# Optimization experiments

Measured on AMD Instinct MI355X. Metric: run time of the kernel, lower is better.

Reference implementation:

```python
import jax, jax.numpy as jnp
import numpy as np

B, S, NV, D = 2, 4096, 8, 256
E = 256          # embedding dim for adaLN conditioning
H = 8            # D / n_head_channels(=32)
HID = 4 * D      # ResLayer MLP hidden
EPS = 1e-5


def setup_inputs() -> dict:
    key = jax.random.key(0)
    ks = jax.random.split(key, 16)
    M = NV * D

    def w(k, shape, scale=0.02):
        return jax.random.normal(k, shape, dtype=jnp.float32) * scale

    mask = jax.random.uniform(ks[0], (B, S, NV)) > 0.2
    mask = mask.at[..., 0].set(True)  # avoid fully-masked rows
    return {
        "x": jax.random.normal(ks[1], (B, S, NV, D), dtype=jnp.float32),
        "emb": jax.random.normal(ks[2], (B, E), dtype=jnp.float32),
        "mask": mask,
        "w_mod1": w(ks[3], (E, 2 * M)), "b_mod1": jnp.zeros((2 * M,), jnp.float32),
        "wq": w(ks[4], (D, D)), "bq": jnp.zeros((D,), jnp.float32),
        "wk": w(ks[5], (D, D)), "bk": jnp.zeros((D,), jnp.float32),
        "wv": w(ks[6], (D, D)), "bv": jnp.zeros((D,), jnp.float32),
        "wo": w(ks[7], (D, D)), "bo": jnp.zeros((D,), jnp.float32),
        "gamma": jnp.full((D,), 1e-6, jnp.float32),
        "w_mod2": w(ks[8], (E, 2 * M)), "b_mod2": jnp.zeros((2 * M,), jnp.float32),
        "w1": w(ks[9], (D, HID)), "b1": jnp.zeros((HID,), jnp.float32),
        "w2": w(ks[10], (HID, D)), "b2": jnp.zeros((D,), jnp.float32),
        "gamma_mlp": jnp.full((D,), 1e-6, jnp.float32),
    }


def _adaln(xin, emb, w, b):
    # AdaptiveLayerNorm over the flattened (NV*D) feature dims,
    # scale/shift conditioned on the embedding.
    b_, s_, nv_, d_ = xin.shape
    xf = xin.reshape(b_, s_, nv_ * d_)
    mu = xf.mean(-1, keepdims=True)
    var = ((xf - mu) ** 2).mean(-1, keepdims=True)
    normed = (xf - mu) * jax.lax.rsqrt(var + EPS)
    scale, shift = jnp.split(emb @ w + b, 2, axis=-1)  # [B, NV*D] each
    out = normed * (1.0 + scale[:, None, :]) + shift[:, None, :]
    return out.reshape(b_, s_, nv_, d_)


def reference(x, emb, mask, w_mod1, b_mod1, wq, bq, wk, bk, wv, bv, wo, bo,
              gamma, w_mod2, b_mod2, w1, b1, w2, b2, gamma_mlp):
    b_, s_, nv_, d_ = x.shape
    hd = d_ // H
    inv_sqrt = jnp.float32(1.0 / np.sqrt(hd))

    # --- attention branch: adaLN -> shape_to_att -> masked attention over variables ---
    h = _adaln(x, emb, w_mod1, b_mod1).reshape(b_ * s_, nv_, d_)
    q = (h @ wq + bq).reshape(b_ * s_, nv_, H, hd)
    k = (h @ wk + bk).reshape(b_ * s_, nv_, H, hd)
    v = (h @ wv + bv).reshape(b_ * s_, nv_, H, hd)
    scores = jnp.einsum('bnhd,bmhd->bhnm', q, k) * inv_sqrt  # [B*S, H, NV, NV]
    mk = mask.reshape(b_ * s_, nv_)
    scores = jnp.where(mk[:, None, None, :], scores, jnp.float32(-1e9))
    attn = jax.nn.softmax(scores, axis=-1)
    o = jnp.einsum('bhnm,bmhd->bnhd', attn, v).reshape(b_ * s_, nv_, d_)
    o = o @ wo + bo
    # dropout is identity at eval; gamma-scaled residual add
    x1 = x + gamma * o.reshape(b_, s_, nv_, d_)

    # --- MLP branch: shape_to_x -> adaLN -> shape_to_att -> ResLayer -> gamma residual ---
    h2 = _adaln(x1, emb, w_mod2, b_mod2)
    m = jax.nn.gelu(h2 @ w1 + b1) @ w2 + b2
    return x1 + gamma_mlp * m
```

## Files before the change

kernel.cpp:

```cpp
#include <hip/hip_runtime.h>
#include <hip/hip_bf16.h>
#include <stdint.h>

#define S_TOK   8192
#define MFEAT   2048

typedef __attribute__((ext_vector_type(4))) float f32x4;
typedef __attribute__((ext_vector_type(8))) short bf16x8;

__device__ __forceinline__ float b2f(uint32_t u) { return __uint_as_float(u << 16); }
__device__ __forceinline__ uint16_t f2b(float f) {
  uint32_t u = __float_as_uint(f);
  uint32_t r = u + 0x7fffu + ((u >> 16) & 1u);
  return (uint16_t)(r >> 16);
}
__device__ __forceinline__ uint32_t pk_bf16(float lo, float hi) {
  uint32_t r;
  asm("v_cvt_pk_bf16_f32 %0, %1, %2" : "=v"(r) : "v"(lo), "v"(hi));
  return r;
}

#define GLP(p) ((__attribute__((address_space(1))) void*)(uintptr_t)(p))
#define LDSP(p) ((__attribute__((address_space(3))) void*)(p))

__global__ __launch_bounds__(256) void k_maskprobe(const uint32_t* __restrict__ m,
                                                   int* __restrict__ flag) {
  __shared__ int s[5];
  const int tid = threadIdx.x;
  if (tid < 5) s[tid] = (tid == 4) ? 0 : 1;
  __syncthreads();
  bool i32ok = true, i8ok = true, f32ok = true, bf16ok = true, saw = false;
  for (int i = tid; i < 1024; i += 256) {
    uint32_t w = m[i];
    if (w > 1u) i32ok = false;
    if (((w | (w >> 8) | (w >> 16) | (w >> 24)) & 0xFEu) != 0) i8ok = false;
    if (w != 0u && w != 0x3F800000u) f32ok = false;
    uint32_t h0 = w & 0xffffu, h1 = w >> 16;
    if ((h0 != 0u && h0 != 0x3F80u) || (h1 != 0u && h1 != 0x3F80u)) bf16ok = false;
    if (w == 0x3F803F80u) saw = true;
  }
  if (!i32ok) s[0] = 0;
  if (!i8ok)  s[1] = 0;
  if (!f32ok) s[2] = 0;
  if (!bf16ok) s[3] = 0;
  if (saw)    s[4] = 1;
  __syncthreads();
  if (tid == 0) {
    int f;
    if (s[0]) f = 0;
    else if (s[1]) f = 1;
    else if (s[3] && s[4]) f = 3;
    else if (s[2]) f = 2;
    else if (s[3]) f = 3;
    else f = 0;
    *flag = f;
  }
}

__global__ __launch_bounds__(256) void k_prep(
    const float* __restrict__ wq, const float* __restrict__ wk,
    const float* __restrict__ wv, const float* __restrict__ wo,
    const float* __restrict__ w1, const float* __restrict__ w2,
    uint16_t* __restrict__ wqf, uint16_t* __restrict__ wof,
    uint16_t* __restrict__ w1f, uint16_t* __restrict__ w2f,
    const void* __restrict__ mask, const int* __restrict__ flag,
    int* __restrict__ mask_i32,
    const float* __restrict__ bq, const float* __restrict__ bk,
    const float* __restrict__ bv, float* __restrict__ biasqkv) {
  int idx = blockIdx.x * 256 + threadIdx.x;
  if (idx < 196608) {
    int o = idx, frag = o >> 9, lane = (o >> 3) & 63, sub = o & 7;
    int ct = frag >> 3, kt = frag & 7;
    int col = ct * 16 + (lane & 15);
    int k = kt * 32 + (lane >> 4) * 8 + sub;
    const float* src = (col < 256) ? wq : (col < 512) ? wk : wv;
    wqf[idx] = f2b(src[k * 256 + (col & 255)]);
  } else if (idx < 262144) {
    int o = idx - 196608, frag = o >> 9, lane = (o >> 3) & 63, sub = o & 7;
    int ct = frag >> 3, kt = frag & 7;
    int col = ct * 16 + (lane & 15);
    int k = kt * 32 + (lane >> 4) * 8 + sub;
    wof[o] = f2b(wo[k * 256 + col]);
  } else if (idx < 524288) {
    int o = idx - 262144, frag = o >> 9, lane = (o >> 3) & 63, sub = o & 7;
    int ct = frag >> 3, kt = frag & 7;
    int col = ct * 16 + (lane & 15);
    int k = kt * 32 + (lane >> 4) * 8 + sub;
    w1f[o] = f2b(w1[k * 1024 + col]);
  } else if (idx < 786432) {
    int o = idx - 524288, frag = o >> 9, lane = (o >> 3) & 63, sub = o & 7;
    int ct = frag >> 5, kt = frag & 31;
    int col = ct * 16 + (lane & 15);
    int k = kt * 32 + (lane >> 4) * 8 + sub;
    w2f[o] = f2b(w2[k * 256 + col]);
  } else if (idx < 851968) {
    int i = idx - 786432;
    int f = *flag;
    int v;
    if (f == 0)      v = ((const int*)mask)[i] != 0;
    else if (f == 1) v = ((const uint8_t*)mask)[i] != 0;
    else if (f == 2) v = ((const uint32_t*)mask)[i] != 0;
    else             v = ((const uint16_t*)mask)[i] != 0;
    mask_i32[i] = v;
  } else if (idx < 852736) {
    int i = idx - 851968;
    biasqkv[i] = (i < 256) ? bq[i] : (i < 512) ? bk[i - 256] : bv[i - 512];
  }
}

__global__ __launch_bounds__(256) void k_mods(
    const float* __restrict__ emb,
    const float* __restrict__ w_mod1, const float* __restrict__ b_mod1,
    const float* __restrict__ w_mod2, const float* __restrict__ b_mod2,
    float* __restrict__ mods) {
  const int j = blockIdx.x * 256 + threadIdx.x;
  const int b = blockIdx.y;
  const int which = blockIdx.z;
  const float* w  = which ? w_mod2 : w_mod1;
  const float* bb = which ? b_mod2 : b_mod1;
  __shared__ float e[256];
  e[threadIdx.x] = emb[b * 256 + threadIdx.x];
  __syncthreads();
  float acc = bb[j];
  for (int kx = 0; kx < 256; kx++) acc += e[kx] * w[(size_t)kx * 4096 + j];
  mods[((size_t)which * 2 + b) * 4096 + j] = acc;
}

__global__ __launch_bounds__(256) void k_qkv(
    const float* __restrict__ x, const float* __restrict__ mods,
    const float* __restrict__ biasqkv, const uint16_t* __restrict__ wqf,
    uint16_t* __restrict__ out, size_t slot, int t0) {
  __shared__ __align__(16) uint16_t As[128 * 256];
  __shared__ float red1[256], red2[256];
  const int tid = threadIdx.x;
  const int l = tid & 63;
  const int wva = tid >> 6;
  const int wr = wva >> 1, wc = wva & 1;
  const int brow = blockIdx.x * 128;
  char* AsB = (char*)As;

  {
    const int r = tid >> 1, ch = (tid & 1) << 7;
    const float4* xp = (const float4*)(x + (size_t)(brow + r) * 256 + ch);
    float s1 = 0.f, s2 = 0.f;
#pragma unroll
    for (int i = 0; i < 32; i++) {
      float4 u = xp[i];
      s1 += u.x + u.y + u.z + u.w;
      s2 += u.x * u.x + u.y * u.y + u.z * u.z + u.w * u.w;
    }
    red1[tid] = s1; red2[tid] = s2;
  }
  __syncthreads();
  {
    const int r = tid >> 1;
    const int base = (r >> 3) << 4;
    float s1 = 0.f, s2 = 0.f;
#pragma unroll
    for (int i = 0; i < 16; i++) { s1 += red1[base + i]; s2 += red2[base + i]; }
    float mean = s1 * (1.f / 2048.f);
    float var = s2 * (1.f / 2048.f) - mean * mean;
    float rs = rsqrtf(var + 1e-5f);
    __syncthreads();
    red1[r] = mean; red2[r] = rs;
  }
  __syncthreads();

#pragma unroll
  for (int it = 0; it < 16; it++) {
    int cidx = it * 256 + tid;
    int row = cidx >> 5, cg = cidx & 31;
    int b = (t0 + ((brow + row) >> 3)) >> 12;
    const float* mo = mods + (size_t)b * 4096 + ((row & 7) << 8) + cg * 8;
    float mean = red1[row], rs = red2[row];
    const float4* xp = (const float4*)(x + (size_t)(brow + row) * 256 + cg * 8);
    float4 u0 = xp[0], u1 = xp[1];
    float4 c0 = *(const float4*)mo,        c1 = *(const float4*)(mo + 4);
    float4 h0 = *(const float4*)(mo + 2048), h1 = *(const float4*)(mo + 2052);
    float v[8] = {u0.x,u0.y,u0.z,u0.w,u1.x,u1.y,u1.z,u1.w};
    float sc[8] = {c0.x,c0.y,c0.z,c0.w,c1.x,c1.y,c1.z,c1.w};
    float sh[8] = {h0.x,h0.y,h0.z,h0.w,h1.x,h1.y,h1.z,h1.w};
    uint32_t w[4];
#pragma unroll
    for (int i = 0; i < 4; i++) {
      float y0 = (v[i*2]   - mean) * rs * (1.f + sc[i*2])   + sh[i*2];
      float y1 = (v[i*2+1] - mean) * rs * (1.f + sc[i*2+1]) + sh[i*2+1];
      w[i] = pk_bf16(y0, y1);
    }
    *(uint4*)(AsB + row * 512 + ((cg * 16) ^ ((row & 7) << 4))) =
        make_uint4(w[0], w[1], w[2], w[3]);
  }
  __syncthreads();

#pragma unroll 1
  for (int nb = 0; nb < 6; nb++) {
    f32x4 acc[4][4];
#pragma unroll
    for (int m = 0; m < 4; m++)
#pragma unroll
      for (int n = 0; n < 4; n++) acc[m][n] = (f32x4)0.f;

#pragma unroll
    for (int kt = 0; kt < 8; kt++) {
      bf16x8 a[4], b[4];
#pragma unroll
      for (int n = 0; n < 4; n++) {
        int ct = nb * 8 + wc * 4 + n;
        b[n] = *(const bf16x8*)(wqf + (((size_t)ct * 8 + kt) * 64 + l) * 8);
      }
#pragma unroll
      for (int m = 0; m < 4; m++) {
        int row = wr * 64 + m * 16 + (l & 15);
        int cb = (kt * 64 + (l >> 4) * 16) ^ ((row & 7) << 4);
        a[m] = *(const bf16x8*)(AsB + row * 512 + cb);
      }
#pragma unroll
      for (int m = 0; m < 4; m++)
#pragma unroll
        for (int n = 0; n < 4; n++)
          acc[m][n] = __builtin_amdgcn_mfma_f32_16x16x32_bf16(a[m], b[n], acc[m][n], 0, 0, 0);
    }

#pragma unroll
    for (int m = 0; m < 4; m++) {
#pragma unroll
      for (int n = 0; n < 4; n++) {
        int col = nb * 128 + wc * 64 + n * 16 + (l & 15);
        float bc = biasqkv[col];
        int b_ = col >> 8, coll = col & 255;
#pragma unroll
        for (int r = 0; r < 4; r++) {
          int row = brow + wr * 64 + m * 16 + (l >> 4) * 4 + r;
          out[(size_t)b_ * slot + (size_t)row * 256 + coll] = f2b(acc[m][n][r] + bc);
        }
      }
    }
  }
}

__global__ __launch_bounds__(256) void k_oproj(
    const uint16_t* __restrict__ A, const uint16_t* __restrict__ wof,
    const float* __restrict__ bias, const float* __restrict__ res,
    const float* __restrict__ gam, uint16_t* __restrict__ x1b,
    float* __restrict__ sbuf) {
  __shared__ __align__(16) uint16_t As[128 * 256];
  __shared__ float sr1[16][2], sr2[16][2];
  const int tid = threadIdx.x;
  const int l = tid & 63;
  const int wva = tid >> 6;
  const int wr = wva >> 1, wc = wva & 1;
  const int brow = blockIdx.x * 128;
  char* AsB = (char*)As;

#pragma unroll
  for (int i = 0; i < 16; i++) {
    int chunk = wva * 16 + i;
    int r = chunk * 2 + (l >> 5);
    int sb = ((l & 31) * 16) ^ ((r & 7) << 4);
    __builtin_amdgcn_global_load_lds(GLP(A + (size_t)(brow + r) * 256 + (sb >> 1)),
                                     LDSP(AsB + chunk * 1024), 16, 0, 0);
  }
  asm volatile("s_waitcnt vmcnt(0)" ::: "memory");
  __syncthreads();

  float ts1[4] = {0.f, 0.f, 0.f, 0.f}, ts2[4] = {0.f, 0.f, 0.f, 0.f};

#pragma unroll 1
  for (int nb = 0; nb < 2; nb++) {
    f32x4 acc[4][4];
#pragma unroll
    for (int m = 0; m < 4; m++)
#pragma unroll
      for (int n = 0; n < 4; n++) acc[m][n] = (f32x4)0.f;

#pragma unroll
    for (int kt = 0; kt < 8; kt++) {
      bf16x8 a[4], b[4];
#pragma unroll
      for (int n = 0; n < 4; n++) {
        int ct = nb * 8 + wc * 4 + n;
        b[n] = *(const bf16x8*)(wof + (((size_t)ct * 8 + kt) * 64 + l) * 8);
      }
#pragma unroll
      for (int m = 0; m < 4; m++) {
        int row = wr * 64 + m * 16 + (l & 15);
        int cb = (kt * 64 + (l >> 4) * 16) ^ ((row & 7) << 4);
        a[m] = *(const bf16x8*)(AsB + row * 512 + cb);
      }
#pragma unroll
      for (int m = 0; m < 4; m++)
#pragma unroll
        for (int n = 0; n < 4; n++)
          acc[m][n] = __builtin_amdgcn_mfma_f32_16x16x32_bf16(a[m], b[n], acc[m][n], 0, 0, 0);
    }

#pragma unroll
    for (int m = 0; m < 4; m++) {
#pragma unroll
      for (int n = 0; n < 4; n++) {
        int col = nb * 128 + wc * 64 + n * 16 + (l & 15);
        float bc = bias[col];
        float gc = gam[col];
#pragma unroll
        for (int r = 0; r < 4; r++) {
          int row = brow + wr * 64 + m * 16 + (l >> 4) * 4 + r;
          float y = res[(size_t)row * 256 + col] + gc * (acc[m][n][r] + bc);
          x1b[(size_t)row * 256 + col] = f2b(y);
          ts1[m] += y; ts2[m] += y * y;
        }
      }
    }
  }

#pragma unroll
  for (int m = 0; m < 4; m++) {
#pragma unroll
    for (int off = 16; off; off >>= 1) {
      ts1[m] += __shfl_xor(ts1[m], off);
      ts2[m] += __shfl_xor(ts2[m], off);
    }
  }
  if ((l & 31) == 0) {
    int h = l >> 5;
#pragma unroll
    for (int m = 0; m < 4; m++) {
      int tok = wr * 8 + 2 * m + h;
      sr1[tok][wc] = ts1[m]; sr2[tok][wc] = ts2[m];
    }
  }
  __syncthreads();
  if (tid < 16) {
    float s1 = sr1[tid][0] + sr1[tid][1];
    float s2 = sr2[tid][0] + sr2[tid][1];
    float mean = s1 * (1.f / 2048.f);
    float var = s2 * (1.f / 2048.f) - mean * mean;
    sbuf[((brow >> 3) + tid) * 2]     = mean;
    sbuf[((brow >> 3) + tid) * 2 + 1] = rsqrtf(var + 1e-5f);
  }
}

__global__ __launch_bounds__(256) void k_mlp(
    const uint16_t* __restrict__ x1b, float* __restrict__ outp,
    const float* __restrict__ mods, const float* __restrict__ sbuf,
    const uint16_t* __restrict__ w1f, const float* __restrict__ b1,
    const uint16_t* __restrict__ w2f, const float* __restrict__ b2,
    const float* __restrict__ gam, int t0) {
  __shared__ __align__(16) uint16_t As[64 * 256];
  __shared__ __align__(16) uint16_t Hs[64 * 128];
  const int tid = threadIdx.x;
  const int l = tid & 63;
  const int w = tid >> 6;
  const int brow = blockIdx.x * 64;
  char* AsB = (char*)As;
  char* HsB = (char*)Hs;

#pragma unroll
  for (int it = 0; it < 8; it++) {
    int cidx = it * 256 + tid;
    int row = cidx >> 5, cg = cidx & 31;
    int gtok = (brow + row) >> 3;
    int b = (t0 + gtok) >> 12;
    const float* mo = mods + (size_t)b * 4096 + ((row & 7) << 8) + cg * 8;
    float mean = sbuf[gtok * 2], rs = sbuf[gtok * 2 + 1];
    uint4 u = *(const uint4*)(x1b + (size_t)(brow + row) * 256 + cg * 8);
    float v[8] = {b2f(u.x & 0xffff), b2f(u.x >> 16), b2f(u.y & 0xffff), b2f(u.y >> 16),
                  b2f(u.z & 0xffff), b2f(u.z >> 16), b2f(u.w & 0xffff), b2f(u.w >> 16)};
    float4 c0 = *(const float4*)mo,        c1 = *(const float4*)(mo + 4);
    float4 h0 = *(const float4*)(mo + 2048), h1 = *(const float4*)(mo + 2052);
    float sc[8] = {c0.x,c0.y,c0.z,c0.w,c1.x,c1.y,c1.z,c1.w};
    float sh[8] = {h0.x,h0.y,h0.z,h0.w,h1.x,h1.y,h1.z,h1.w};
    uint32_t wv[4];
#pragma unroll
    for (int i = 0; i < 4; i++) {
      float y0 = (v[i*2]   - mean) * rs * (1.f + sc[i*2])   + sh[i*2];
      float y1 = (v[i*2+1] - mean) * rs * (1.f + sc[i*2+1]) + sh[i*2+1];
      wv[i] = pk_bf16(y0, y1);
    }
    *(uint4*)(AsB + row * 512 + ((cg * 16) ^ ((row & 7) << 4))) =
        make_uint4(wv[0], wv[1], wv[2], wv[3]);
  }

  f32x4 acc2[4][4];
#pragma unroll
  for (int m = 0; m < 4; m++)
#pragma unroll
    for (int n = 0; n < 4; n++) acc2[m][n] = (f32x4)0.f;
  __syncthreads();

#pragma unroll 1
  for (int c = 0; c < 8; c++) {
    f32x4 acc1[2][4];
#pragma unroll
    for (int n = 0; n < 2; n++)
#pragma unroll
      for (int m = 0; m < 4; m++) acc1[n][m] = (f32x4)0.f;
#pragma unroll
    for (int kt = 0; kt < 8; kt++) {
      bf16x8 a[4], b[2];
#pragma unroll
      for (int n = 0; n < 2; n++) {
        int ct = c * 8 + w * 2 + n;
        b[n] = *(const bf16x8*)(w1f + (((size_t)ct * 8 + kt) * 64 + l) * 8);
      }
#pragma unroll
      for (int m = 0; m < 4; m++) {
        int row = m * 16 + (l & 15);
        int cb = (kt * 64 + (l >> 4) * 16) ^ ((row & 7) << 4);
        a[m] = *(const bf16x8*)(AsB + row * 512 + cb);
      }
#pragma unroll
      for (int n = 0; n < 2; n++)
#pragma unroll
        for (int m = 0; m < 4; m++)
          acc1[n][m] = __builtin_amdgcn_mfma_f32_16x16x32_bf16(b[n], a[m], acc1[n][m], 0, 0, 0);
    }
    __syncthreads();
#pragma unroll
    for (int n = 0; n < 2; n++) {
      int hb = w * 32 + n * 16 + (l >> 4) * 4;
      float4 bb = *(const float4*)(b1 + c * 128 + hb);
#pragma unroll
      for (int m = 0; m < 4; m++) {
        int token = m * 16 + (l & 15);
        float g[4];
#pragma unroll
        for (int j = 0; j < 4; j++) {
          float y = acc1[n][m][j] + ((const float*)&bb)[j];
          float t = __expf(-1.702f * y);
          g[j] = __fdividef(y, 1.f + t);
        }
        int byte = (token * 256 + hb * 2) ^ ((token & 7) << 4);
        *(uint2*)(HsB + byte) = make_uint2(pk_bf16(g[0], g[1]), pk_bf16(g[2], g[3]));
      }
    }
    __syncthreads();
#pragma unroll
    for (int kt = 0; kt < 4; kt++) {
      bf16x8 h[4], b[4];
#pragma unroll
      for (int n = 0; n < 4; n++) {
        int ct = w * 4 + n;
        int kidx = c * 4 + kt;
        b[n] = *(const bf16x8*)(w2f + (((size_t)ct * 32 + kidx) * 64 + l) * 8);
      }
#pragma unroll
      for (int m = 0; m < 4; m++) {
        int row = m * 16 + (l & 15);
        int cb = (kt * 64 + (l >> 4) * 16) ^ ((row & 7) << 4);
        h[m] = *(const bf16x8*)(HsB + row * 256 + cb);
      }
#pragma unroll
      for (int m = 0; m < 4; m++)
#pragma unroll
        for (int n = 0; n < 4; n++)
          acc2[m][n] = __builtin_amdgcn_mfma_f32_16x16x32_bf16(h[m], b[n], acc2[m][n], 0, 0, 0);
    }
  }

#pragma unroll
  for (int m = 0; m < 4; m++) {
#pragma unroll
    for (int n = 0; n < 4; n++) {
      int col = w * 64 + n * 16 + (l & 15);
      float bc = b2[col];
      float gc = gam[col];
#pragma unroll
      for (int r = 0; r < 4; r++) {
        int row = brow + m * 16 + (l >> 4) * 4 + r;
        float y = b2f(x1b[(size_t)row * 256 + col]) + gc * (acc2[m][n][r] + bc);
        outp[(size_t)row * 256 + col] = y;
      }
    }
  }
}

__global__ __launch_bounds__(256) void k_attn(
    const uint16_t* __restrict__ q, const uint16_t* __restrict__ k,
    const uint16_t* __restrict__ v, const int* __restrict__ mask,
    uint16_t* __restrict__ o) {
  __shared__ __align__(16) uint16_t kk[4][2048];
  __shared__ __align__(16) uint16_t vv[4][2048];
  const int l = threadIdx.x & 63;
  const int wva = threadIdx.x >> 6;
  const int t = blockIdx.x * 4 + wva;

#pragma unroll
  for (int c = 0; c < 4; c++) {
    __builtin_amdgcn_global_load_lds(GLP(k + (size_t)t * 2048 + c * 512 + l * 8),
                                     LDSP(&kk[wva][c * 512]), 16, 0, 0);
    __builtin_amdgcn_global_load_lds(GLP(v + (size_t)t * 2048 + c * 512 + l * 8),
                                     LDSP(&vv[wva][c * 512]), 16, 0, 0);
  }

  const int h = l >> 3, n = l & 7;
  const uint4* qp = (const uint4*)(q + (size_t)t * 2048 + n * 256 + h * 32);
  float qf[32];
#pragma unroll
  for (int c = 0; c < 4; c++) {
    uint4 u = qp[c];
    qf[c*8+0]=b2f(u.x & 0xffff); qf[c*8+1]=b2f(u.x >> 16);
    qf[c*8+2]=b2f(u.y & 0xffff); qf[c*8+3]=b2f(u.y >> 16);
    qf[c*8+4]=b2f(u.z & 0xffff); qf[c*8+5]=b2f(u.z >> 16);
    qf[c*8+6]=b2f(u.w & 0xffff); qf[c*8+7]=b2f(u.w >> 16);
  }
  asm volatile("s_waitcnt vmcnt(0)" ::: "memory");

  float s[8];
#pragma unroll
  for (int m = 0; m < 8; m++) {
    const uint4* kp = (const uint4*)&kk[wva][m * 256 + h * 32];
    float acc = 0.f;
#pragma unroll
    for (int c = 0; c < 4; c++) {
      uint4 u = kp[c];
      acc += qf[c*8+0]*b2f(u.x & 0xffff) + qf[c*8+1]*b2f(u.x >> 16)
           + qf[c*8+2]*b2f(u.y & 0xffff) + qf[c*8+3]*b2f(u.y >> 16)
           + qf[c*8+4]*b2f(u.z & 0xffff) + qf[c*8+5]*b2f(u.z >> 16)
           + qf[c*8+6]*b2f(u.w & 0xffff) + qf[c*8+7]*b2f(u.w >> 16);
    }
    s[m] = acc * 0.17677669529663687f;
  }
  const int* mk = mask + (size_t)t * 8;
  float mx = -1e30f;
#pragma unroll
  for (int m = 0; m < 8; m++) { s[m] = mk[m] ? s[m] : -1e9f; mx = fmaxf(mx, s[m]); }
  float p[8], sum = 0.f;
#pragma unroll
  for (int m = 0; m < 8; m++) { p[m] = __expf(s[m] - mx); sum += p[m]; }
  float inv = __fdividef(1.f, sum);
  float of[32];
#pragma unroll
  for (int d = 0; d < 32; d++) of[d] = 0.f;
#pragma unroll
  for (int m = 0; m < 8; m++) {
    float pm = p[m] * inv;
    const uint4* vp = (const uint4*)&vv[wva][m * 256 + h * 32];
#pragma unroll
    for (int c = 0; c < 4; c++) {
      uint4 u = vp[c];
      of[c*8+0]+=pm*b2f(u.x & 0xffff); of[c*8+1]+=pm*b2f(u.x >> 16);
      of[c*8+2]+=pm*b2f(u.y & 0xffff); of[c*8+3]+=pm*b2f(u.y >> 16);
      of[c*8+4]+=pm*b2f(u.z & 0xffff); of[c*8+5]+=pm*b2f(u.z >> 16);
      of[c*8+6]+=pm*b2f(u.w & 0xffff); of[c*8+7]+=pm*b2f(u.w >> 16);
    }
  }
  uint16_t* op = o + (size_t)t * 2048 + n * 256 + h * 32;
#pragma unroll
  for (int c = 0; c < 4; c++) {
    ((uint4*)op)[c] = make_uint4(pk_bf16(of[c*8+0], of[c*8+1]),
                                 pk_bf16(of[c*8+2], of[c*8+3]),
                                 pk_bf16(of[c*8+4], of[c*8+5]),
                                 pk_bf16(of[c*8+6], of[c*8+7]));
  }
}

extern "C" void kernel_launch(void* const* d_in, const int* in_sizes, int n_in,
                              void* d_out, int out_size, void* d_ws, size_t ws_size,
                              hipStream_t stream) {
  const float* x      = (const float*)d_in[0];
  const float* emb    = (const float*)d_in[1];
  const void*  mask   = d_in[2];
  const float* w_mod1 = (const float*)d_in[3];
  const float* b_mod1 = (const float*)d_in[4];
  const float* wq = (const float*)d_in[5];
  const float* bq = (const float*)d_in[6];
  const float* wk = (const float*)d_in[7];
  const float* bk = (const float*)d_in[8];
  const float* wv = (const float*)d_in[9];
  const float* bv = (const float*)d_in[10];
  const float* wo = (const float*)d_in[11];
  const float* bo = (const float*)d_in[12];
  const float* gamma     = (const float*)d_in[13];
  const float* w_mod2    = (const float*)d_in[14];
  const float* b_mod2    = (const float*)d_in[15];
  const float* w1 = (const float*)d_in[16];
  const float* b1 = (const float*)d_in[17];
  const float* w2 = (const float*)d_in[18];
  const float* b2 = (const float*)d_in[19];
  const float* gamma_mlp = (const float*)d_in[20];

  char* ws = (char*)d_ws;
  float*    mods = (float*)ws;
  uint16_t* wqf = (uint16_t*)(ws + 65536);
  uint16_t* wof = wqf + 196608;
  uint16_t* w1f = wof + 65536;
  uint16_t* w2f = w1f + 262144;
  int*      mask_i32 = (int*)(w2f + 262144);
  int*      flag = mask_i32 + 65536;
  float*    biasqkv = (float*)(flag + 1);
  float*    sbuf = biasqkv + 768;
  uint16_t* slots = (uint16_t*)(ws + (2u << 20));
  float*    xout = (float*)d_out;

  size_t budget = (ws_size > (3u << 20)) ? ws_size - (2u << 20) : 0;
  int maxtok = (int)(budget / 20480);
  int chunk_tokens = 16;
  for (int c = 8192; c >= 16; c >>= 1) { if (c <= maxtok) { chunk_tokens = c; break; } }
  const int nchunks = S_TOK / chunk_tokens;
  const int crows = chunk_tokens * 8;
  const size_t slot = (size_t)crows * 256;
  uint16_t* C0 = slots;
  uint16_t* C1 = C0 + slot;
  uint16_t* C4 = C0 + 4 * slot;

  k_maskprobe<<<dim3(1), 256, 0, stream>>>((const uint32_t*)mask, flag);
  k_prep<<<dim3(3331), 256, 0, stream>>>(wq, wk, wv, wo, w1, w2, wqf, wof, w1f, w2f,
                                         mask, flag, mask_i32, bq, bk, bv, biasqkv);
  k_mods<<<dim3(16, 2, 2), 256, 0, stream>>>(emb, w_mod1, b_mod1, w_mod2, b_mod2, mods);

  for (int c = 0; c < nchunks; c++) {
    const int t0 = c * chunk_tokens;
    const size_t eo = (size_t)t0 * MFEAT;
    const float* xc = x + eo;
    float* outc = xout + eo;
    k_qkv<<<dim3(crows / 128), 256, 0, stream>>>(xc, mods, biasqkv, wqf, C1, slot, t0);
    k_attn<<<dim3(chunk_tokens / 4), 256, 0, stream>>>(C1, C1 + slot, C1 + 2 * slot,
                                                       mask_i32 + (size_t)t0 * 8, C0);
    k_oproj<<<dim3(crows / 128), 256, 0, stream>>>(C0, wof, bo, xc, gamma, C4, sbuf);
    k_mlp<<<dim3(crows / 64), 256, 0, stream>>>(C4, outc, mods + 2 * 4096, sbuf,
                                                w1f, b1, w2f, b2, gamma_mlp, t0);
  }
}
```

Before: 288.9 us.

## Fuse variable attention into output projection kernel via shared LDS tile

Merges the attention kernel and the output-projection kernel into one kernel. Each 64-row block (8 tokens) loads K and V into LDS, computes masked softmax attention per wave, and writes the attention output back into the same LDS buffer in a swizzled layout. The MFMA O-projection then reads that buffer directly, which removes the global write and re-read of the attention output and one launch per chunk. In exchange the projection tile shrinks from 128 to 64 rows with 4 waves splitting columns, so wof weight reuse per block drops and the grid doubles.

Result: slower. 317.6 us (+9.9%).

```diff
diff --git a/kernel.cpp b/kernel.cpp
--- a/kernel.cpp
+++ b/kernel.cpp
@@ -238,73 +238,132 @@
   }
 }
 
-__global__ __launch_bounds__(256) void k_oproj(
-    const uint16_t* __restrict__ A, const uint16_t* __restrict__ wof,
-    const float* __restrict__ bias, const float* __restrict__ res,
-    const float* __restrict__ gam, uint16_t* __restrict__ x1b,
-    float* __restrict__ sbuf) {
-  __shared__ __align__(16) uint16_t As[128 * 256];
-  __shared__ float sr1[16][2], sr2[16][2];
+__global__ __launch_bounds__(256) void k_oav(
+    const uint16_t* __restrict__ q, const uint16_t* __restrict__ kk,
+    const uint16_t* __restrict__ vv, const int* __restrict__ mask,
+    const uint16_t* __restrict__ wof, const float* __restrict__ bias,
+    const float* __restrict__ res, const float* __restrict__ gam,
+    uint16_t* __restrict__ x1b, float* __restrict__ sbuf) {
+  __shared__ __align__(16) uint16_t As[8 * 4096];
+  __shared__ float sr1[8][4], sr2[8][4];
   const int tid = threadIdx.x;
   const int l = tid & 63;
-  const int wva = tid >> 6;
-  const int wr = wva >> 1, wc = wva & 1;
-  const int brow = blockIdx.x * 128;
+  const int w = tid >> 6;
+  const int brow = blockIdx.x * 64;
+  const int T0 = brow >> 3;
   char* AsB = (char*)As;
 
 #pragma unroll
   for (int i = 0; i < 16; i++) {
-    int chunk = wva * 16 + i;
-    int r = chunk * 2 + (l >> 5);
-    int sb = ((l & 31) * 16) ^ ((r & 7) << 4);
-    __builtin_amdgcn_global_load_lds(GLP(A + (size_t)(brow + r) * 256 + (sb >> 1)),
-                                     LDSP(AsB + chunk * 1024), 16, 0, 0);
+    int chunk = w * 16 + i;
+    int tl = chunk >> 3, sub = chunk & 7;
+    const uint16_t* src = ((sub < 4) ? kk : vv) + (size_t)(T0 + tl) * 2048 + (sub & 3) * 512;
+    __builtin_amdgcn_global_load_lds(GLP(src + l * 8), LDSP(AsB + chunk * 1024), 16, 0, 0);
   }
   asm volatile("s_waitcnt vmcnt(0)" ::: "memory");
+
+  const int h = l >> 3, n = l & 7;
+#pragma unroll 1
+  for (int tl2 = 0; tl2 < 2; tl2++) {
+    const int tl = w * 2 + tl2;
+    const uint4* qp = (const uint4*)(q + (size_t)(T0 + tl) * 2048 + n * 256 + h * 32);
+    float qf[32];
+#pragma unroll
+    for (int c = 0; c < 4; c++) {
+      uint4 u = qp[c];
+      qf[c*8+0]=b2f(u.x & 0xffff); qf[c*8+1]=b2f(u.x >> 16);
+      qf[c*8+2]=b2f(u.y & 0xffff); qf[c*8+3]=b2f(u.y >> 16);
+      qf[c*8+4]=b2f(u.z & 0xffff); qf[c*8+5]=b2f(u.z >> 16);
+      qf[c*8+6]=b2f(u.w & 0xffff); qf[c*8+7]=b2f(u.w >> 16);
+    }
+    float s[8];
+#pragma unroll
+    for (int m = 0; m < 8; m++) {
+      const uint4* kp = (const uint4*)(AsB + tl * 8192 + m * 512 + h * 64);
+      float acc = 0.f;
+#pragma unroll
+      for (int c = 0; c < 4; c++) {
+        uint4 u = kp[c];
+        acc += qf[c*8+0]*b2f(u.x & 0xffff) + qf[c*8+1]*b2f(u.x >> 16)
+             + qf[c*8+2]*b2f(u.y & 0xffff) + qf[c*8+3]*b2f(u.y >> 16)
+             + qf[c*8+4]*b2f(u.z & 0xffff) + qf[c*8+5]*b2f(u.z >> 16)
+             + qf[c*8+6]*b2f(u.w & 0xffff) + qf[c*8+7]*b2f(u.w >> 16);
+      }
+      s[m] = acc * 0.17677669529663687f;
+    }
+    const int* mk = mask + (size_t)(T0 + tl) * 8;
+    float mx = -1e30f;
+#pragma unroll
+    for (int m = 0; m < 8; m++) { s[m] = mk[m] ? s[m] : -1e9f; mx = fmaxf(mx, s[m]); }
+    float p[8], sum = 0.f;
+#pragma unroll
+    for (int m = 0; m < 8; m++) { p[m] = __expf(s[m] - mx); sum += p[m]; }
+    float inv = __fdividef(1.f, sum);
+    float of[32];
+#pragma unroll
+    for (int d = 0; d < 32; d++) of[d] = 0.f;
+#pragma unroll
+    for (int m = 0; m < 8; m++) {
+      float pm = p[m] * inv;
+      const uint4* vp = (const uint4*)(AsB + tl * 8192 + 4096 + m * 512 + h * 64);
+#pragma unroll
+      for (int c = 0; c < 4; c++) {
+        uint4 u = vp[c];
+        of[c*8+0]+=pm*b2f(u.x & 0xffff); of[c*8+1]+=pm*b2f(u.x >> 16);
+        of[c*8+2]+=pm*b2f(u.y & 0xffff); of[c*8+3]+=pm*b2f(u.y >> 16);
+        of[c*8+4]+=pm*b2f(u.z & 0xffff); of[c*8+5]+=pm*b2f(u.z >> 16);
+        of[c*8+6]+=pm*b2f(u.w & 0xffff); of[c*8+7]+=pm*b2f(u.w >> 16);
+      }
+    }
+#pragma unroll
+    for (int c = 0; c < 4; c++) {
+      int byte = tl * 8192 + n * 512 + ((h * 64 + c * 16) ^ (n << 4));
+      *(uint4*)(AsB + byte) = make_uint4(pk_bf16(of[c*8+0], of[c*8+1]),
+                                         pk_bf16(of[c*8+2], of[c*8+3]),
+                                         pk_bf16(of[c*8+4], of[c*8+5]),
+                                         pk_bf16(of[c*8+6], of[c*8+7]));
+    }
+  }
   __syncthreads();
 
   float ts1[4] = {0.f, 0.f, 0.f, 0.f}, ts2[4] = {0.f, 0.f, 0.f, 0.f};
-
 #pragma unroll 1
   for (int nb = 0; nb < 2; nb++) {
-    f32x4 acc[4][4];
-#pragma unroll
-    for (int m = 0; m < 4; m++)
-#pragma unroll
-      for (int n = 0; n < 4; n++) acc[m][n] = (f32x4)0.f;
-
+    f32x4 acc[4][2];
+#pragma unroll
+    for (int m = 0; m < 4; m++) { acc[m][0] = (f32x4)0.f; acc[m][1] = (f32x4)0.f; }
 #pragma unroll
     for (int kt = 0; kt < 8; kt++) {
-      bf16x8 a[4], b[4];
-#pragma unroll
-      for (int n = 0; n < 4; n++) {
-        int ct = nb * 8 + wc * 4 + n;
-        b[n] = *(const bf16x8*)(wof + (((size_t)ct * 8 + kt) * 64 + l) * 8);
+      bf16x8 a[4], b[2];
+#pragma unroll
+      for (int n2 = 0; n2 < 2; n2++) {
+        int ct = w * 4 + nb * 2 + n2;
+        b[n2] = *(const bf16x8*)(wof + (((size_t)ct * 8 + kt) * 64 + l) * 8);
       }
 #pragma unroll
       for (int m = 0; m < 4; m++) {
-        int row = wr * 64 + m * 16 + (l & 15);
-        int cb = (kt * 64 + (l >> 4) * 16) ^ ((row & 7) << 4);
-        a[m] = *(const bf16x8*)(AsB + row * 512 + cb);
+        int row = m * 16 + (l & 15);
+        int byte = (row >> 3) * 8192 + (row & 7) * 512 +
+                   ((kt * 64 + (l >> 4) * 16) ^ ((row & 7) << 4));
+        a[m] = *(const bf16x8*)(AsB + byte);
       }
 #pragma unroll
       for (int m = 0; m < 4; m++)
 #pragma unroll
-        for (int n = 0; n < 4; n++)
-          acc[m][n] = __builtin_amdgcn_mfma_f32_16x16x32_bf16(a[m], b[n], acc[m][n], 0, 0, 0);
-    }
-
+        for (int n2 = 0; n2 < 2; n2++)
+          acc[m][n2] = __builtin_amdgcn_mfma_f32_16x16x32_bf16(a[m], b[n2], acc[m][n2], 0, 0, 0);
+    }
 #pragma unroll
     for (int m = 0; m < 4; m++) {
 #pragma unroll
-      for (int n = 0; n < 4; n++) {
-        int col = nb * 128 + wc * 64 + n * 16 + (l & 15);
+      for (int n2 = 0; n2 < 2; n2++) {
+        int col = w * 64 + nb * 32 + n2 * 16 + (l & 15);
         float bc = bias[col];
         float gc = gam[col];
 #pragma unroll
         for (int r = 0; r < 4; r++) {
-          int row = brow + wr * 64 + m * 16 + (l >> 4) * 4 + r;
-          float y = res[(size_t)row * 256 + col] + gc * (acc[m][n][r] + bc);
+          int row = brow + m * 16 + (l >> 4) * 4 + r;
+          float y = res[(size_t)row * 256 + col] + gc * (acc[m][n2][r] + bc);
           x1b[(size_t)row * 256 + col] = f2b(y);
           ts1[m] += y; ts2[m] += y * y;
         }
@@ -321,21 +380,21 @@
     }
   }
   if ((l & 31) == 0) {
-    int h = l >> 5;
+    int hh = l >> 5;
 #pragma unroll
     for (int m = 0; m < 4; m++) {
-      int tok = wr * 8 + 2 * m + h;
-      sr1[tok][wc] = ts1[m]; sr2[tok][wc] = ts2[m];
-    }
-  }
-  __syncthreads();
-  if (tid < 16) {
-    float s1 = sr1[tid][0] + sr1[tid][1];
-    float s2 = sr2[tid][0] + sr2[tid][1];
+      int tok = 2 * m + hh;
+      sr1[tok][w] = ts1[m]; sr2[tok][w] = ts2[m];
+    }
+  }
+  __syncthreads();
+  if (tid < 8) {
+    float s1 = sr1[tid][0] + sr1[tid][1] + sr1[tid][2] + sr1[tid][3];
+    float s2 = sr2[tid][0] + sr2[tid][1] + sr2[tid][2] + sr2[tid][3];
     float mean = s1 * (1.f / 2048.f);
     float var = s2 * (1.f / 2048.f) - mean * mean;
-    sbuf[((brow >> 3) + tid) * 2]     = mean;
-    sbuf[((brow >> 3) + tid) * 2 + 1] = rsqrtf(var + 1e-5f);
+    sbuf[(T0 + tid) * 2]     = mean;
+    sbuf[(T0 + tid) * 2 + 1] = rsqrtf(var + 1e-5f);
   }
 }
 
@@ -471,86 +530,6 @@
         outp[(size_t)row * 256 + col] = y;
       }
     }
-  }
-}
-
-__global__ __launch_bounds__(256) void k_attn(
-    const uint16_t* __restrict__ q, const uint16_t* __restrict__ k,
-    const uint16_t* __restrict__ v, const int* __restrict__ mask,
-    uint16_t* __restrict__ o) {
-  __shared__ __align__(16) uint16_t kk[4][2048];
-  __shared__ __align__(16) uint16_t vv[4][2048];
-  const int l = threadIdx.x & 63;
-  const int wva = threadIdx.x >> 6;
-  const int t = blockIdx.x * 4 + wva;
-
-#pragma unroll
-  for (int c = 0; c < 4; c++) {
-    __builtin_amdgcn_global_load_lds(GLP(k + (size_t)t * 2048 + c * 512 + l * 8),
-                                     LDSP(&kk[wva][c * 512]), 16, 0, 0);
-    __builtin_amdgcn_global_load_lds(GLP(v + (size_t)t * 2048 + c * 512 + l * 8),
-                                     LDSP(&vv[wva][c * 512]), 16, 0, 0);
-  }
-
-  const int h = l >> 3, n = l & 7;
-  const uint4* qp = (const uint4*)(q + (size_t)t * 2048 + n * 256 + h * 32);
-  float qf[32];
-#pragma unroll
-  for (int c = 0; c < 4; c++) {
-    uint4 u = qp[c];
-    qf[c*8+0]=b2f(u.x & 0xffff); qf[c*8+1]=b2f(u.x >> 16);
-    qf[c*8+2]=b2f(u.y & 0xffff); qf[c*8+3]=b2f(u.y >> 16);
-    qf[c*8+4]=b2f(u.z & 0xffff); qf[c*8+5]=b2f(u.z >> 16);
-    qf[c*8+6]=b2f(u.w & 0xffff); qf[c*8+7]=b2f(u.w >> 16);
-  }
-  asm volatile("s_waitcnt vmcnt(0)" ::: "memory");
-
-  float s[8];
-#pragma unroll
-  for (int m = 0; m < 8; m++) {
-    const uint4* kp = (const uint4*)&kk[wva][m * 256 + h * 32];
-    float acc = 0.f;
-#pragma unroll
-    for (int c = 0; c < 4; c++) {
-      uint4 u = kp[c];
-      acc += qf[c*8+0]*b2f(u.x & 0xffff) + qf[c*8+1]*b2f(u.x >> 16)
-           + qf[c*8+2]*b2f(u.y & 0xffff) + qf[c*8+3]*b2f(u.y >> 16)
-           + qf[c*8+4]*b2f(u.z & 0xffff) + qf[c*8+5]*b2f(u.z >> 16)
-           + qf[c*8+6]*b2f(u.w & 0xffff) + qf[c*8+7]*b2f(u.w >> 16);
-    }
-    s[m] = acc * 0.17677669529663687f;
-  }
-  const int* mk = mask + (size_t)t * 8;
-  float mx = -1e30f;
-#pragma unroll
-  for (int m = 0; m < 8; m++) { s[m] = mk[m] ? s[m] : -1e9f; mx = fmaxf(mx, s[m]); }
-  float p[8], sum = 0.f;
-#pragma unroll
-  for (int m = 0; m < 8; m++) { p[m] = __expf(s[m] - mx); sum += p[m]; }
-  float inv = __fdividef(1.f, sum);
-  float of[32];
-#pragma unroll
-  for (int d = 0; d < 32; d++) of[d] = 0.f;
-#pragma unroll
-  for (int m = 0; m < 8; m++) {
-    float pm = p[m] * inv;
-    const uint4* vp = (const uint4*)&vv[wva][m * 256 + h * 32];
-#pragma unroll
-    for (int c = 0; c < 4; c++) {
-      uint4 u = vp[c];
-      of[c*8+0]+=pm*b2f(u.x & 0xffff); of[c*8+1]+=pm*b2f(u.x >> 16);
-      of[c*8+2]+=pm*b2f(u.y & 0xffff); of[c*8+3]+=pm*b2f(u.y >> 16);
-      of[c*8+4]+=pm*b2f(u.z & 0xffff); of[c*8+5]+=pm*b2f(u.z >> 16);
-      of[c*8+6]+=pm*b2f(u.w & 0xffff); of[c*8+7]+=pm*b2f(u.w >> 16);
-    }
-  }
-  uint16_t* op = o + (size_t)t * 2048 + n * 256 + h * 32;
-#pragma unroll
-  for (int c = 0; c < 4; c++) {
-    ((uint4*)op)[c] = make_uint4(pk_bf16(of[c*8+0], of[c*8+1]),
-                                 pk_bf16(of[c*8+2], of[c*8+3]),
-                                 pk_bf16(of[c*8+4], of[c*8+5]),
-                                 pk_bf16(of[c*8+6], of[c*8+7]));
   }
 }
 
@@ -599,9 +578,8 @@
   const int nchunks = S_TOK / chunk_tokens;
   const int crows = chunk_tokens * 8;
   const size_t slot = (size_t)crows * 256;
-  uint16_t* C0 = slots;
-  uint16_t* C1 = C0 + slot;
-  uint16_t* C4 = C0 + 4 * slot;
+  uint16_t* C1 = slots + slot;
+  uint16_t* C4 = slots + 4 * slot;
 
   k_maskprobe<<<dim3(1), 256, 0, stream>>>((const uint32_t*)mask, flag);
   k_prep<<<dim3(3331), 256, 0, stream>>>(wq, wk, wv, wo, w1, w2, wqf, wof, w1f, w2f,
@@ -614,9 +592,9 @@
     const float* xc = x + eo;
     float* outc = xout + eo;
     k_qkv<<<dim3(crows / 128), 256, 0, stream>>>(xc, mods, biasqkv, wqf, C1, slot, t0);
-    k_attn<<<dim3(chunk_tokens / 4), 256, 0, stream>>>(C1, C1 + slot, C1 + 2 * slot,
-                                                       mask_i32 + (size_t)t0 * 8, C0);
-    k_oproj<<<dim3(crows / 128), 256, 0, stream>>>(C0, wof, bo, xc, gamma, C4, sbuf);
+    k_oav<<<dim3(crows / 64), 256, 0, stream>>>(C1, C1 + slot, C1 + 2 * slot,
+                                                mask_i32 + (size_t)t0 * 8,
+                                                wof, bo, xc, gamma, C4, sbuf);
     k_mlp<<<dim3(crows / 64), 256, 0, stream>>>(C4, outc, mods + 2 * 4096, sbuf,
                                                 w1f, b1, w2f, b2, gamma_mlp, t0);
   }
```
